# Kernel optimization log

Measured on AMD Instinct MI355X. Metric: run time of the kernel, lower is better.

Reference implementation:

```python
import jax, jax.numpy as jnp
import numpy as np

N_NODES = 100000


def setup_inputs() -> dict:
    key = jax.random.key(0)
    k1, k2, k3, k4 = jax.random.split(key, 4)
    h = jax.random.normal(k1, (N_NODES, 128), dtype=jnp.float32)
    src = jax.random.randint(k2, (1600000,), 0, N_NODES, dtype=jnp.int32)
    dst = jax.random.randint(k3, (1600000,), 0, N_NODES, dtype=jnp.int32)
    # Linear params (PyTorch default init scale ~ 1/sqrt(in_feats))
    W = jax.random.normal(k4, (128, 128), dtype=jnp.float32) * (1.0 / np.sqrt(128.0))
    b = jnp.zeros((128,), dtype=jnp.float32)
    return {"h": h, "src": src, "dst": dst, "W": W, "b": b}


def reference(h, src, dst, W, b):
    # fn.copy_src: gather source-node features per edge  [E, F]
    msgs = h[src]
    # fn.sum: scatter-add messages into destination nodes  [N, F]
    agg = jax.ops.segment_sum(msgs, dst, num_segments=h.shape[0])
    # NodeUpdateModule: linear + relu
    out = agg @ W.T + b
    return jax.nn.relu(out)
```

## Files before the change

### kernel.cpp

```cpp
#include <hip/hip_runtime.h>

#define F     128
#define NPB   128
#define NPBS  7
#define CAP   6144
#define NBMAX 1024
#define SPLIT 4
#define NPG   32
#define ECAP  1024
#define BR    64
#define KC    32

typedef short bf16x8 __attribute__((ext_vector_type(8)));
typedef float f32x4  __attribute__((ext_vector_type(4)));

__device__ __forceinline__ unsigned short f32_to_bf16_rne(float x) {
    unsigned u = __float_as_uint(x);
    u += 0x7fffu + ((u >> 16) & 1u);
    return (unsigned short)(u >> 16);
}
__device__ __forceinline__ float bf16_to_f32(unsigned short u) {
    return __uint_as_float((unsigned)u << 16);
}

__global__ __launch_bounds__(256) void conv_w_kernel(
        const float* __restrict__ Wf, unsigned short* __restrict__ Wb, int n4) {
    int i = blockIdx.x * blockDim.x + threadIdx.x;
    if (i < n4) {
        float4 v = *(const float4*)(Wf + 4 * (long)i);
        ushort4 o;
        o.x = f32_to_bf16_rne(v.x);
        o.y = f32_to_bf16_rne(v.y);
        o.z = f32_to_bf16_rne(v.z);
        o.w = f32_to_bf16_rne(v.w);
        *(ushort4*)(Wb + 4 * (long)i) = o;
    }
}

__global__ __launch_bounds__(256) void gemm_h_kernel(
        const float* __restrict__ h,
        const unsigned short* __restrict__ Wb,
        unsigned short* __restrict__ hp,
        int n_rows) {
    const int wave = (blockIdx.x * 256 + threadIdx.x) >> 6;
    const int lane = threadIdx.x & 63;
    const int m0 = wave * 16;
    if (m0 >= n_rows) return;
    const int mn   = lane & 15;
    const int quad = lane >> 4;

    const int rowc = min(m0 + mn, n_rows - 1);
    const float* arow = h + (long)rowc * F + quad * 8;

    bf16x8 afr[4];
    #pragma unroll
    for (int kk = 0; kk < 4; ++kk) {
        float4 p0 = *(const float4*)(arow + kk * 32);
        float4 p1 = *(const float4*)(arow + kk * 32 + 4);
        bf16x8 f;
        f[0] = (short)f32_to_bf16_rne(p0.x);
        f[1] = (short)f32_to_bf16_rne(p0.y);
        f[2] = (short)f32_to_bf16_rne(p0.z);
        f[3] = (short)f32_to_bf16_rne(p0.w);
        f[4] = (short)f32_to_bf16_rne(p1.x);
        f[5] = (short)f32_to_bf16_rne(p1.y);
        f[6] = (short)f32_to_bf16_rne(p1.z);
        f[7] = (short)f32_to_bf16_rne(p1.w);
        afr[kk] = f;
    }

    f32x4 acc[8];
    #pragma unroll
    for (int t = 0; t < 8; ++t) acc[t] = (f32x4){0.f, 0.f, 0.f, 0.f};

    #pragma unroll
    for (int kk = 0; kk < 4; ++kk) {
        #pragma unroll
        for (int t = 0; t < 8; ++t) {
            const unsigned short* wp = Wb + (long)(t * 16 + mn) * F + kk * 32 + quad * 8;
            bf16x8 bfr = *(const bf16x8*)wp;
            acc[t] = __builtin_amdgcn_mfma_f32_16x16x32_bf16(afr[kk], bfr, acc[t], 0, 0, 0);
        }
    }

    #pragma unroll
    for (int t = 0; t < 8; ++t) {
        const int col = t * 16 + mn;
        #pragma unroll
        for (int r = 0; r < 4; ++r) {
            const int orow = m0 + quad * 4 + r;
            if (orow < n_rows)
                hp[(long)orow * F + col] = f32_to_bf16_rne(acc[t][r]);
        }
    }
}

__global__ __launch_bounds__(256) void build_buckets_kernel(
        const int* __restrict__ src,
        const int* __restrict__ dst,
        const unsigned short* __restrict__ hp,
        int* __restrict__ bcnt,
        int* __restrict__ bpool,
        float* __restrict__ out,
        int n_edges, int NB) {
    __shared__ int hist[NBMAX];
    __shared__ int basep[NBMAX];

    const int per = (n_edges + gridDim.x - 1) / gridDim.x;
    const int lo = blockIdx.x * per;
    const int hi = min(n_edges, lo + per);
    const int tid = threadIdx.x;

    for (int i = tid; i < NB; i += 256) hist[i] = 0;
    __syncthreads();

    for (int i = lo + tid; i < hi; i += 256)
        atomicAdd(&hist[dst[i] >> NPBS], 1);
    __syncthreads();

    for (int i = tid; i < NB; i += 256) {
        int c = hist[i];
        basep[i] = c ? atomicAdd(&bcnt[i], c) : 0;
        hist[i] = 0;
    }
    __syncthreads();

    for (int i = lo + tid; i < hi; i += 256) {
        int d = dst[i], s = src[i];
        int bk = d >> NPBS;
        int p = atomicAdd(&hist[bk], 1);
        long idx = (long)basep[bk] + p;
        if (idx < CAP) {
            bpool[(long)bk * CAP + idx] = ((d & (NPB - 1)) << 20) | s;
        } else {
            float* o = out + (long)d * F;
            const unsigned short* hr = hp + (long)s * F;
            for (int k = 0; k < F; ++k) unsafeAtomicAdd(o + k, bf16_to_f32(hr[k]));
        }
    }
}

__global__ __launch_bounds__(256) void bucket_gather_kernel(
        const unsigned short* __restrict__ hp,
        const int* __restrict__ bcnt,
        const int* __restrict__ bpool,
        const float* __restrict__ bias,
        float* __restrict__ out,
        int n_nodes) {
    __shared__ int ecnt[NPG];
    __shared__ int eofs[NPG];
    __shared__ int epos[NPG];
    __shared__ int elist[ECAP];
    __shared__ int sflag;

    const int bkt = blockIdx.x >> 2;
    const int qr  = blockIdx.x & 3;
    const int q0  = qr * NPG;
    const int nb0 = (bkt << NPBS) + q0;
    const int tid = threadIdx.x;

    const int total = bcnt[bkt];
    const int count = min(total, CAP);
    const int* bp = bpool + (long)bkt * CAP;

    if (tid < NPG) ecnt[tid] = 0;
    if (tid == 0) sflag = 0;
    __syncthreads();

    for (int i = tid; i < count; i += 256) {
        int nl = (bp[i] >> 20) - q0;
        if ((unsigned)nl < NPG) atomicAdd(&ecnt[nl], 1);
    }
    __syncthreads();

    if (tid < NPG) {
        int a = ecnt[tid];
        int s = a;
        #pragma unroll
        for (int d = 1; d < NPG; d <<= 1) {
            int t = __shfl_up(s, d);
            if (tid >= d) s += t;
        }
        eofs[tid] = s - a;
        epos[tid] = s - a;
    }
    __syncthreads();

    for (int i = tid; i < count; i += 256) {
        int e = bp[i];
        int nl = (e >> 20) - q0;
        if ((unsigned)nl < NPG) {
            int p = atomicAdd(&epos[nl], 1);
            int s = e & 0xFFFFF;
            if (p < ECAP) {
                elist[p] = s;
            } else {
                sflag = 1;
                float* o = out + ((long)((bkt << NPBS) + (e >> 20))) * F;
                const unsigned short* hr = hp + (long)s * F;
                for (int k = tid & 0; k < F; ++k)
                    unsafeAtomicAdd(o + k, bf16_to_f32(hr[k]));
            }
        }
    }
    __syncthreads();

    const int lane = tid & 63;
    const int w = tid >> 6;
    const bool ovf = (total > CAP) || (sflag != 0);
    const float2 bv = *(const float2*)(bias + (lane << 1));

    for (int nl = w; nl < NPG; nl += 4) {
        int n = nb0 + nl;
        if (n >= n_nodes) break;
        const int beg = eofs[nl];
        const int dend = min(beg + ecnt[nl], ECAP);

        float ax = 0.f, ay = 0.f;
        for (int i = beg; i < dend; i += 8) {
            unsigned v[8]; bool val[8];
            #pragma unroll
            for (int j = 0; j < 8; ++j) {
                val[j] = (i + j) < dend;
                int sid = elist[val[j] ? i + j : beg];
                v[j] = *(const unsigned*)(hp + ((long)sid << NPBS) + (lane << 1));
            }
            #pragma unroll
            for (int j = 0; j < 8; ++j) {
                if (val[j]) {
                    ax += __uint_as_float(v[j] << 16);
                    ay += __uint_as_float(v[j] & 0xffff0000u);
                }
            }
        }

        float* o = out + ((long)n << NPBS) + (lane << 1);
        if (ovf) {
            ax += unsafeAtomicAdd(o, 0.f);
            ay += unsafeAtomicAdd(o + 1, 0.f);
        }
        float rx = fmaxf(ax + bv.x, 0.f);
        float ry = fmaxf(ay + bv.y, 0.f);
        *(float2*)o = make_float2(rx, ry);
    }
}

__global__ void scatter_add_kernel(const float* __restrict__ h,
                                   const int* __restrict__ src,
                                   const int* __restrict__ dst,
                                   float* __restrict__ agg,
                                   long total) {
    long stride = (long)gridDim.x * blockDim.x;
    for (long i = (long)blockIdx.x * blockDim.x + threadIdx.x; i < total; i += stride) {
        int e    = (int)(i >> 5);
        int lane = (int)(i & 31);
        int s = src[e];
        int d = dst[e];
        float4 v = *(const float4*)(h + (long)s * F + (lane << 2));
        float* o = agg + (long)d * F + (lane << 2);
        unsafeAtomicAdd(o + 0, v.x);
        unsafeAtomicAdd(o + 1, v.y);
        unsafeAtomicAdd(o + 2, v.z);
        unsafeAtomicAdd(o + 3, v.w);
    }
}

__global__ __launch_bounds__(256) void gemm_bias_relu_inplace(
        float* __restrict__ out,
        const float* __restrict__ W,
        const float* __restrict__ bias,
        int n_rows) {
    __shared__ __align__(16) float a_t[KC][BR + 4];
    __shared__ __align__(16) float w_t[KC][F + 4];
    const int tid = threadIdx.x;
    const int tx = tid & 15;
    const int ty = tid >> 4;
    const int row0 = blockIdx.x * BR;
    float acc[4][8];
    #pragma unroll
    for (int i = 0; i < 4; ++i)
        #pragma unroll
        for (int j = 0; j < 8; ++j) acc[i][j] = 0.f;
    for (int kc = 0; kc < F; kc += KC) {
        #pragma unroll
        for (int p = 0; p < 2; ++p) {
            int q = tid + p * 256, r = q >> 3, kq = q & 7;
            int row = row0 + r;
            float4 v = make_float4(0.f, 0.f, 0.f, 0.f);
            if (row < n_rows) v = *(const float4*)(out + (long)row * F + kc + (kq << 2));
            a_t[kq * 4 + 0][r] = v.x; a_t[kq * 4 + 1][r] = v.y;
            a_t[kq * 4 + 2][r] = v.z; a_t[kq * 4 + 3][r] = v.w;
        }
        #pragma unroll
        for (int p = 0; p < 4; ++p) {
            int q = tid + p * 256, j = q >> 3, kq = q & 7;
            float4 v = *(const float4*)(W + (long)j * F + kc + (kq << 2));
            w_t[kq * 4 + 0][j] = v.x; w_t[kq * 4 + 1][j] = v.y;
            w_t[kq * 4 + 2][j] = v.z; w_t[kq * 4 + 3][j] = v.w;
        }
        __syncthreads();
        #pragma unroll
        for (int k = 0; k < KC; ++k) {
            float4 av = *(const float4*)&a_t[k][ty << 2];
            float4 w0 = *(const float4*)&w_t[k][tx << 2];
            float4 w1 = *(const float4*)&w_t[k][64 + (tx << 2)];
            float a4[4] = {av.x, av.y, av.z, av.w};
            float wv[8] = {w0.x, w0.y, w0.z, w0.w, w1.x, w1.y, w1.z, w1.w};
            #pragma unroll
            for (int i = 0; i < 4; ++i)
                #pragma unroll
                for (int j = 0; j < 8; ++j) acc[i][j] += a4[i] * wv[j];
        }
        __syncthreads();
    }
    float4 b0 = *(const float4*)(bias + (tx << 2));
    float4 b1 = *(const float4*)(bias + 64 + (tx << 2));
    #pragma unroll
    for (int i = 0; i < 4; ++i) {
        int row = row0 + (ty << 2) + i;
        if (row < n_rows) {
            float4 r0, r1;
            r0.x = fmaxf(acc[i][0] + b0.x, 0.f); r0.y = fmaxf(acc[i][1] + b0.y, 0.f);
            r0.z = fmaxf(acc[i][2] + b0.z, 0.f); r0.w = fmaxf(acc[i][3] + b0.w, 0.f);
            r1.x = fmaxf(acc[i][4] + b1.x, 0.f); r1.y = fmaxf(acc[i][5] + b1.y, 0.f);
            r1.z = fmaxf(acc[i][6] + b1.z, 0.f); r1.w = fmaxf(acc[i][7] + b1.w, 0.f);
            *(float4*)(out + (long)row * F + (tx << 2)) = r0;
            *(float4*)(out + (long)row * F + 64 + (tx << 2)) = r1;
        }
    }
}

extern "C" void kernel_launch(void* const* d_in, const int* in_sizes, int n_in,
                              void* d_out, int out_size, void* d_ws, size_t ws_size,
                              hipStream_t stream) {
    const float* h   = (const float*)d_in[0];
    const int*   src = (const int*)d_in[1];
    const int*   dst = (const int*)d_in[2];
    const float* W   = (const float*)d_in[3];
    const float* b   = (const float*)d_in[4];
    float* out = (float*)d_out;

    const int n_nodes = in_sizes[0] / F;
    const int n_edges = in_sizes[1];
    const int NB = (n_nodes + NPB - 1) >> NPBS;

    const size_t off_bcnt  = 0;
    const size_t off_bpool = 4096;
    const size_t off_hp    = off_bpool + (size_t)NB * CAP * sizeof(int);
    const size_t off_wb    = off_hp + (size_t)n_nodes * F * sizeof(unsigned short);
    const size_t need      = off_wb + (size_t)F * F * sizeof(unsigned short);

    if (ws_size >= need && n_nodes < (1 << 20) && NB <= NBMAX) {
        int* bcnt  = (int*)((char*)d_ws + off_bcnt);
        int* bpool = (int*)((char*)d_ws + off_bpool);
        unsigned short* hp = (unsigned short*)((char*)d_ws + off_hp);
        unsigned short* Wb = (unsigned short*)((char*)d_ws + off_wb);

        hipMemsetAsync(bcnt, 0, (size_t)NB * sizeof(int), stream);
        hipMemsetAsync(out, 0, (size_t)out_size * sizeof(float), stream);

        conv_w_kernel<<<(F * F / 4 + 255) / 256, 256, 0, stream>>>(W, Wb, F * F / 4);

        const int ggrid = (n_nodes + 63) / 64;
        gemm_h_kernel<<<ggrid, 256, 0, stream>>>(h, Wb, hp, n_nodes);

        build_buckets_kernel<<<512, 256, 0, stream>>>(
            src, dst, hp, bcnt, bpool, out, n_edges, NB);

        bucket_gather_kernel<<<NB * SPLIT, 256, 0, stream>>>(
            hp, bcnt, bpool, b, out, n_nodes);
    } else {
        hipMemsetAsync(out, 0, (size_t)out_size * sizeof(float), stream);
        scatter_add_kernel<<<16384, 256, 0, stream>>>(
            h, src, dst, out, (long)n_edges * 32);
        const int gblocks = (n_nodes + BR - 1) / BR;
        gemm_bias_relu_inplace<<<gblocks, 256, 0, stream>>>(out, W, b, n_nodes);
    }
}
```

Before: 263.2 us.

## Replace bucketed edge sort with per-node fixed-capacity adjacency pool

Bucketed edge lists and the LDS-based regrouping are replaced by a direct per-destination pool of up to 40 source slots, filled with global atomics on per-node counters. Rare excess edges go to a small global overflow list, which each node scans linearly in the gather. Each wave then handles 16 consecutive nodes and reads their neighbor rows directly. This drops the 51 MB memset of the output, the two-pass histogram and the per-block LDS staging, in exchange for random scattered pool writes and 1.6M global atomics. Overflow beyond the list capacity would be silently dropped, and a large overflow would make the per-node scan costly.

```diff
diff --git a/kernel.cpp b/kernel.cpp
--- a/kernel.cpp
+++ b/kernel.cpp
@@ -1,15 +1,11 @@
 #include <hip/hip_runtime.h>
 
-#define F     128
-#define NPB   128
-#define NPBS  7
-#define CAP   6144
-#define NBMAX 1024
-#define SPLIT 4
-#define NPG   32
-#define ECAP  1024
-#define BR    64
-#define KC    32
+#define F      128
+#define DCAP   40
+#define OVFCAP 32768
+#define NPW    16
+#define BR     64
+#define KC     32
 
 typedef short bf16x8 __attribute__((ext_vector_type(8)));
 typedef float f32x4  __attribute__((ext_vector_type(4)));
@@ -95,150 +91,90 @@
     }
 }
 
-__global__ __launch_bounds__(256) void build_buckets_kernel(
+__global__ __launch_bounds__(256) void build_pool_kernel(
         const int* __restrict__ src,
         const int* __restrict__ dst,
+        int* __restrict__ cnt,
+        int* __restrict__ pool,
+        int* __restrict__ ovf,
+        int n_edges) {
+    const int stride = gridDim.x * 256;
+    for (int i = blockIdx.x * 256 + threadIdx.x; i < n_edges; i += stride) {
+        int d = dst[i], s = src[i];
+        int p = atomicAdd(&cnt[d], 1);
+        if (p < DCAP) {
+            pool[(long)d * DCAP + p] = s;
+        } else {
+            int q = atomicAdd(&ovf[0], 1);
+            if (q < OVFCAP) { ovf[1 + 2 * q] = d; ovf[2 + 2 * q] = s; }
+        }
+    }
+}
+
+__global__ __launch_bounds__(256) void node_gather_kernel(
         const unsigned short* __restrict__ hp,
-        int* __restrict__ bcnt,
-        int* __restrict__ bpool,
-        float* __restrict__ out,
-        int n_edges, int NB) {
-    __shared__ int hist[NBMAX];
-    __shared__ int basep[NBMAX];
-
-    const int per = (n_edges + gridDim.x - 1) / gridDim.x;
-    const int lo = blockIdx.x * per;
-    const int hi = min(n_edges, lo + per);
-    const int tid = threadIdx.x;
-
-    for (int i = tid; i < NB; i += 256) hist[i] = 0;
-    __syncthreads();
-
-    for (int i = lo + tid; i < hi; i += 256)
-        atomicAdd(&hist[dst[i] >> NPBS], 1);
-    __syncthreads();
-
-    for (int i = tid; i < NB; i += 256) {
-        int c = hist[i];
-        basep[i] = c ? atomicAdd(&bcnt[i], c) : 0;
-        hist[i] = 0;
-    }
-    __syncthreads();
-
-    for (int i = lo + tid; i < hi; i += 256) {
-        int d = dst[i], s = src[i];
-        int bk = d >> NPBS;
-        int p = atomicAdd(&hist[bk], 1);
-        long idx = (long)basep[bk] + p;
-        if (idx < CAP) {
-            bpool[(long)bk * CAP + idx] = ((d & (NPB - 1)) << 20) | s;
-        } else {
-            float* o = out + (long)d * F;
-            const unsigned short* hr = hp + (long)s * F;
-            for (int k = 0; k < F; ++k) unsafeAtomicAdd(o + k, bf16_to_f32(hr[k]));
-        }
-    }
-}
-
-__global__ __launch_bounds__(256) void bucket_gather_kernel(
-        const unsigned short* __restrict__ hp,
-        const int* __restrict__ bcnt,
-        const int* __restrict__ bpool,
+        const int* __restrict__ cnt,
+        const int* __restrict__ pool,
+        const int* __restrict__ ovf,
         const float* __restrict__ bias,
         float* __restrict__ out,
         int n_nodes) {
-    __shared__ int ecnt[NPG];
-    __shared__ int eofs[NPG];
-    __shared__ int epos[NPG];
-    __shared__ int elist[ECAP];
-    __shared__ int sflag;
-
-    const int bkt = blockIdx.x >> 2;
-    const int qr  = blockIdx.x & 3;
-    const int q0  = qr * NPG;
-    const int nb0 = (bkt << NPBS) + q0;
-    const int tid = threadIdx.x;
-
-    const int total = bcnt[bkt];
-    const int count = min(total, CAP);
-    const int* bp = bpool + (long)bkt * CAP;
-
-    if (tid < NPG) ecnt[tid] = 0;
-    if (tid == 0) sflag = 0;
-    __syncthreads();
-
-    for (int i = tid; i < count; i += 256) {
-        int nl = (bp[i] >> 20) - q0;
-        if ((unsigned)nl < NPG) atomicAdd(&ecnt[nl], 1);
-    }
-    __syncthreads();
-
-    if (tid < NPG) {
-        int a = ecnt[tid];
-        int s = a;
-        #pragma unroll
-        for (int d = 1; d < NPG; d <<= 1) {
-            int t = __shfl_up(s, d);
-            if (tid >= d) s += t;
-        }
-        eofs[tid] = s - a;
-        epos[tid] = s - a;
-    }
-    __syncthreads();
-
-    for (int i = tid; i < count; i += 256) {
-        int e = bp[i];
-        int nl = (e >> 20) - q0;
-        if ((unsigned)nl < NPG) {
-            int p = atomicAdd(&epos[nl], 1);
-            int s = e & 0xFFFFF;
-            if (p < ECAP) {
-                elist[p] = s;
-            } else {
-                sflag = 1;
-                float* o = out + ((long)((bkt << NPBS) + (e >> 20))) * F;
-                const unsigned short* hr = hp + (long)s * F;
-                for (int k = tid & 0; k < F; ++k)
-                    unsafeAtomicAdd(o + k, bf16_to_f32(hr[k]));
-            }
-        }
-    }
-    __syncthreads();
-
-    const int lane = tid & 63;
-    const int w = tid >> 6;
-    const bool ovf = (total > CAP) || (sflag != 0);
+    const int lane = threadIdx.x & 63;
+    const int wv = __builtin_amdgcn_readfirstlane(threadIdx.x >> 6);
+    const int n0 = (blockIdx.x * 4 + wv) * NPW;
+    const unsigned fofs = lane << 1;
     const float2 bv = *(const float2*)(bias + (lane << 1));
-
-    for (int nl = w; nl < NPG; nl += 4) {
-        int n = nb0 + nl;
-        if (n >= n_nodes) break;
-        const int beg = eofs[nl];
-        const int dend = min(beg + ecnt[nl], ECAP);
+    const int novf = ovf[0];
+
+    for (int t = 0; t < NPW; ++t) {
+        const int n = n0 + t;
+        if (n >= n_nodes) return;
+        const int deg = min(cnt[n], DCAP);
+        const int* pl = pool + (long)n * DCAP;
 
         float ax = 0.f, ay = 0.f;
-        for (int i = beg; i < dend; i += 8) {
-            unsigned v[8]; bool val[8];
+        int i = 0;
+        for (; i + 8 <= deg; i += 8) {
+            unsigned v[8];
             #pragma unroll
             for (int j = 0; j < 8; ++j) {
-                val[j] = (i + j) < dend;
-                int sid = elist[val[j] ? i + j : beg];
-                v[j] = *(const unsigned*)(hp + ((long)sid << NPBS) + (lane << 1));
+                int s = pl[i + j];
+                v[j] = *(const unsigned*)(hp + ((long)s << 7) + fofs);
             }
             #pragma unroll
             for (int j = 0; j < 8; ++j) {
-                if (val[j]) {
-                    ax += __uint_as_float(v[j] << 16);
-                    ay += __uint_as_float(v[j] & 0xffff0000u);
+                ax += __uint_as_float(v[j] << 16);
+                ay += __uint_as_float(v[j] & 0xffff0000u);
+            }
+        }
+        if (i < deg) {
+            unsigned v[8];
+            #pragma unroll
+            for (int j = 0; j < 8; ++j) {
+                int idx = i + j;
+                int sr = pl[idx];
+                int s = (idx < deg) ? sr : n_nodes;
+                v[j] = *(const unsigned*)(hp + ((long)s << 7) + fofs);
+            }
+            #pragma unroll
+            for (int j = 0; j < 8; ++j) {
+                ax += __uint_as_float(v[j] << 16);
+                ay += __uint_as_float(v[j] & 0xffff0000u);
+            }
+        }
+        if (novf > 0) {
+            int ne = min(novf, OVFCAP);
+            for (int k = 0; k < ne; ++k) {
+                if (ovf[1 + 2 * k] == n) {
+                    int s = ovf[2 + 2 * k];
+                    unsigned vv = *(const unsigned*)(hp + ((long)s << 7) + fofs);
+                    ax += __uint_as_float(vv << 16);
+                    ay += __uint_as_float(vv & 0xffff0000u);
                 }
             }
         }
 
-        float* o = out + ((long)n << NPBS) + (lane << 1);
-        if (ovf) {
-            ax += unsafeAtomicAdd(o, 0.f);
-            ay += unsafeAtomicAdd(o + 1, 0.f);
-        }
+        float* o = out + ((long)n << 7) + (lane << 1);
         float rx = fmaxf(ax + bv.x, 0.f);
         float ry = fmaxf(ay + bv.y, 0.f);
         *(float2*)o = make_float2(rx, ry);
@@ -342,33 +278,37 @@
 
     const int n_nodes = in_sizes[0] / F;
     const int n_edges = in_sizes[1];
-    const int NB = (n_nodes + NPB - 1) >> NPBS;
-
-    const size_t off_bcnt  = 0;
-    const size_t off_bpool = 4096;
-    const size_t off_hp    = off_bpool + (size_t)NB * CAP * sizeof(int);
-    const size_t off_wb    = off_hp + (size_t)n_nodes * F * sizeof(unsigned short);
-    const size_t need      = off_wb + (size_t)F * F * sizeof(unsigned short);
-
-    if (ws_size >= need && n_nodes < (1 << 20) && NB <= NBMAX) {
-        int* bcnt  = (int*)((char*)d_ws + off_bcnt);
-        int* bpool = (int*)((char*)d_ws + off_bpool);
+
+    auto al16 = [](size_t x) { return (x + 15) & ~(size_t)15; };
+    const size_t off_cnt  = 0;
+    const size_t off_ovf  = al16((size_t)n_nodes * 4);
+    const size_t off_pool = al16(off_ovf + 4 + (size_t)OVFCAP * 8);
+    const size_t off_hp   = al16(off_pool + (size_t)n_nodes * DCAP * 4);
+    const size_t off_wb   = al16(off_hp + (size_t)(n_nodes + 1) * F * 2);
+    const size_t need     = off_wb + (size_t)F * F * 2;
+
+    if (ws_size >= need && n_nodes > 0) {
+        int* cnt  = (int*)((char*)d_ws + off_cnt);
+        int* ovf  = (int*)((char*)d_ws + off_ovf);
+        int* pool = (int*)((char*)d_ws + off_pool);
         unsigned short* hp = (unsigned short*)((char*)d_ws + off_hp);
         unsigned short* Wb = (unsigned short*)((char*)d_ws + off_wb);
 
-        hipMemsetAsync(bcnt, 0, (size_t)NB * sizeof(int), stream);
-        hipMemsetAsync(out, 0, (size_t)out_size * sizeof(float), stream);
+        hipMemsetAsync(cnt, 0, (size_t)n_nodes * 4, stream);
+        hipMemsetAsync(ovf, 0, 4, stream);
+        hipMemsetAsync(hp + (size_t)n_nodes * F, 0, (size_t)F * 2, stream);
 
         conv_w_kernel<<<(F * F / 4 + 255) / 256, 256, 0, stream>>>(W, Wb, F * F / 4);
 
-        const int ggrid = (n_nodes + 63) / 64;
-        gemm_h_kernel<<<ggrid, 256, 0, stream>>>(h, Wb, hp, n_nodes);
-
-        build_buckets_kernel<<<512, 256, 0, stream>>>(
-            src, dst, hp, bcnt, bpool, out, n_edges, NB);
-
-        bucket_gather_kernel<<<NB * SPLIT, 256, 0, stream>>>(
-            hp, bcnt, bpool, b, out, n_nodes);
+        gemm_h_kernel<<<(n_nodes + 63) / 64, 256, 0, stream>>>(h, Wb, hp, n_nodes);
+
+        int bgrid = (n_edges + 255) / 256;
+        if (bgrid > 2048) bgrid = 2048;
+        if (bgrid < 1) bgrid = 1;
+        build_pool_kernel<<<bgrid, 256, 0, stream>>>(src, dst, cnt, pool, ovf, n_edges);
+
+        node_gather_kernel<<<(n_nodes + 4 * NPW - 1) / (4 * NPW), 256, 0, stream>>>(
+            hp, cnt, pool, ovf, b, out, n_nodes);
     } else {
         hipMemsetAsync(out, 0, (size_t)out_size * sizeof(float), stream);
         scatter_add_kernel<<<16384, 256, 0, stream>>>(
```

New measurement: 363.7 us. 1.38x slower.
